# Performance work log

Hardware: AMD Instinct MI355X
Metric: run time of the kernel (lower is better)

Reference implementation:

```python
import jax, jax.numpy as jnp
import numpy as np

B, C, N, K, E = 8, 64, 4096, 16, 64
EPS = 1e-5


def _bn(h, gamma, beta, axes):
    # BatchNorm in training mode: stats over batch+spatial axes, per channel (dim 1)
    m = jnp.mean(h, axis=axes, keepdims=True)
    v = jnp.var(h, axis=axes, keepdims=True)
    shape = (1, -1) + (1,) * (h.ndim - 2)
    return gamma.reshape(shape) * (h - m) * jax.lax.rsqrt(v + EPS) + beta.reshape(shape)


def setup_inputs() -> dict:
    key = jax.random.key(0)
    ks = jax.random.split(key, 8)
    x = jax.random.normal(ks[0], (B, C, N), dtype=jnp.float32)
    idx = jax.random.randint(ks[1], (B, N, K), 0, N, dtype=jnp.int32)
    s1 = 1.0 / np.sqrt(C)
    s2 = 1.0 / np.sqrt(E)
    return {
        "x": x,
        "idx": idx,
        "W1": jax.random.normal(ks[2], (E, C), jnp.float32) * s1,
        "b1": jnp.zeros((E,), jnp.float32),
        "g1": jnp.ones((E,), jnp.float32),
        "be1": jnp.zeros((E,), jnp.float32),
        "W2": jax.random.normal(ks[3], (E, E), jnp.float32) * s2,
        "b2": jnp.zeros((E,), jnp.float32),
        "g2": jnp.ones((E,), jnp.float32),
        "be2": jnp.zeros((E,), jnp.float32),
        "W3": jax.random.normal(ks[4], (E, E), jnp.float32) * s2,
        "b3": jnp.zeros((E,), jnp.float32),
        "g3": jnp.ones((E,), jnp.float32),
        "be3": jnp.zeros((E,), jnp.float32),
    }


def reference(x, idx, W1, b1, g1, be1, W2, b2, g2, be2, W3, b3, g3, be3):
    # gather kNN neighbor features: x[b, :, idx[b]] -> (B, C, N, K)
    nn_feat = jax.vmap(lambda xb, ib: xb[:, ib])(x, idx)
    # edge features: neighbor - center
    h = nn_feat - x[..., None]                                   # (B, C, N, K)
    # Conv2DBlock: two 1x1 conv + BN + ReLU layers
    h = jnp.einsum('bcnk,oc->bonk', h, W1) + b1[:, None, None]
    h = jax.nn.relu(_bn(h, g1, be1, (0, 2, 3)))
    h = jnp.einsum('bcnk,oc->bonk', h, W2) + b2[:, None, None]
    h = jax.nn.relu(_bn(h, g2, be2, (0, 2, 3)))
    # max over neighbors
    h = jnp.max(h, axis=-1)                                      # (B, E, N)
    # Conv1DBlock: 1x1 conv + BN + ReLU
    h = jnp.einsum('bcn,oc->bon', h, W3) + b3[:, None]
    h = jax.nn.relu(_bn(h, g3, be3, (0, 2)))
    return h
```

## Files before the change

kernel.cpp:

```cpp
#include <hip/hip_runtime.h>

#define EPSBN 1e-5f
#define CNT1 524288.0f
#define CNT3 32768.0f
#define NREP 16

typedef short v8s __attribute__((ext_vector_type(8)));
typedef float v16f __attribute__((ext_vector_type(16)));

__device__ __forceinline__ unsigned short f2bf(float f) {
  union { float f; unsigned u; } v; v.f = f;
  unsigned u = v.u;
  u += 0x7fffu + ((u >> 16) & 1u);
  return (unsigned short)(u >> 16);
}
__device__ __forceinline__ unsigned pack2bf(float a, float b) {
  return (unsigned)f2bf(a) | ((unsigned)f2bf(b) << 16);
}
__device__ __forceinline__ float bflo(unsigned u) {
  union { unsigned u; float f; } v; v.u = u << 16; return v.f;
}
__device__ __forceinline__ float bfhi(unsigned u) {
  union { unsigned u; float f; } v; v.u = u & 0xffff0000u; return v.f;
}

__global__ __launch_bounds__(256) void prep(
    const float* __restrict__ x, const float* __restrict__ W1,
    unsigned short* __restrict__ y) {
  __shared__ unsigned short ldsX[64 * 72];
  int blk = blockIdx.x, t = threadIdx.x;
  int b = blk >> 6, n0 = (blk & 63) << 6;
  int tn = t & 63, cg = t >> 6;
#pragma unroll
  for (int i = 0; i < 16; ++i) {
    int c = cg * 16 + i;
    ldsX[tn * 72 + c] = f2bf(x[(((size_t)(b * 64 + c)) << 12) + n0 + tn]);
  }
  __syncthreads();
  int lane = t & 63, w = t >> 6;
  int l31 = lane & 31, lh = lane >> 5;
  int ot = w & 1, ph = w >> 1;
  int o = ot * 32 + l31;
  v16f acc;
#pragma unroll
  for (int i = 0; i < 16; ++i) acc[i] = 0.f;
#pragma unroll
  for (int ks = 0; ks < 4; ++ks) {
    const float* wrow = W1 + o * 64 + ks * 16 + lh * 8;
    float4 wa = *((const float4*)wrow);
    float4 wb = *((const float4*)(wrow + 4));
    v8s wf; unsigned* wu = (unsigned*)&wf;
    wu[0] = pack2bf(wa.x, wa.y); wu[1] = pack2bf(wa.z, wa.w);
    wu[2] = pack2bf(wb.x, wb.y); wu[3] = pack2bf(wb.z, wb.w);
    v8s af = *((const v8s*)&ldsX[(ph * 32 + l31) * 72 + ks * 16 + lh * 8]);
    acc = __builtin_amdgcn_mfma_f32_32x32x16_bf16(af, wf, acc, 0, 0, 0);
  }
#pragma unroll
  for (int i = 0; i < 16; ++i) {
    int row = (i & 3) + ((i >> 2) << 3) + (lh << 2);
    int pt = (b << 12) + n0 + ph * 32 + row;
    y[pt * 64 + o] = f2bf(acc[i]);
  }
}

__global__ __launch_bounds__(256) void p1_stats(
    const unsigned short* __restrict__ y, const int* __restrict__ idx,
    float* __restrict__ S1) {
  __shared__ float bs[64], bq[64];
  int t = threadIdx.x;
  if (t < 64) { bs[t] = 0.f; bq[t] = 0.f; }
  __syncthreads();
  int blk = blockIdx.x;
  int batch = blk & 7, bi = blk >> 3;
  int w = t >> 6, lane = t & 63;
  int ch = (lane & 7) << 3, eg = lane >> 3;
  int ebase = (batch << 16) + bi * 512 + w * 128;
  float ss[8], sq[8];
#pragma unroll
  for (int k = 0; k < 8; ++k) { ss[k] = 0.f; sq[k] = 0.f; }
  for (int it = 0; it < 16; ++it) {
    int p = ebase + it * 8 + eg;
    int j = idx[p];
    int site = p >> 4;
    uint4 uj = *((const uint4*)(y + (((size_t)((batch << 12) + j)) << 6) + ch));
    uint4 ui = *((const uint4*)(y + (((size_t)site) << 6) + ch));
    const unsigned* aj = (const unsigned*)&uj;
    const unsigned* ai = (const unsigned*)&ui;
#pragma unroll
    for (int d = 0; d < 4; ++d) {
      float d0 = bflo(aj[d]) - bflo(ai[d]);
      float d1 = bfhi(aj[d]) - bfhi(ai[d]);
      ss[2 * d] += d0; sq[2 * d] += d0 * d0;
      ss[2 * d + 1] += d1; sq[2 * d + 1] += d1 * d1;
    }
  }
#pragma unroll
  for (int k = 0; k < 8; ++k) {
    ss[k] += __shfl_xor(ss[k], 8);  sq[k] += __shfl_xor(sq[k], 8);
    ss[k] += __shfl_xor(ss[k], 16); sq[k] += __shfl_xor(sq[k], 16);
    ss[k] += __shfl_xor(ss[k], 32); sq[k] += __shfl_xor(sq[k], 32);
  }
  if (lane < 8) {
#pragma unroll
    for (int k = 0; k < 8; ++k) {
      atomicAdd(&bs[ch + k], ss[k]);
      atomicAdd(&bq[ch + k], sq[k]);
    }
  }
  __syncthreads();
  int rep = (blk >> 3) & (NREP - 1);
  if (t < 64) atomicAdd(&S1[rep * 128 + t], bs[t]);
  else if (t < 128) atomicAdd(&S1[rep * 128 + t], bq[t - 64]);
}

__global__ __launch_bounds__(256) void p2_main(
    const unsigned short* __restrict__ y, const int* __restrict__ idx,
    const float* __restrict__ W2f,
    const float* __restrict__ g1, const float* __restrict__ be1,
    const float* __restrict__ S1,
    unsigned short* __restrict__ mnb, unsigned short* __restrict__ mxb,
    float* __restrict__ S2) {
  __shared__ float bs[64], bq[64];
  __shared__ __align__(16) float lA[64];
  __shared__ __align__(16) float lC[64];
  int t = threadIdx.x;
  if (t < 64) {
    bs[t] = 0.f; bq[t] = 0.f;
    float s = 0.f, q = 0.f;
#pragma unroll
    for (int r = 0; r < NREP; ++r) { s += S1[r * 128 + t]; q += S1[r * 128 + 64 + t]; }
    float mean = s / CNT1;
    float var = q / CNT1 - mean * mean;
    float a = g1[t] * rsqrtf(var + EPSBN);
    lA[t] = a; lC[t] = be1[t] - mean * a;
  }
  __syncthreads();
  int blk = blockIdx.x;
  int batch = blk & 7, bi = blk >> 3;
  int w = t >> 6, lane = t & 63;
  int l31 = lane & 31, lh = lane >> 5;
  v8s w2[2][4];
#pragma unroll
  for (int s = 0; s < 2; ++s)
#pragma unroll
    for (int ks = 0; ks < 4; ++ks) {
      const float* wr = W2f + (s * 32 + l31) * 64 + ks * 16 + lh * 8;
      float4 wa = *((const float4*)wr);
      float4 wb = *((const float4*)(wr + 4));
      unsigned* wu = (unsigned*)&w2[s][ks];
      wu[0] = pack2bf(wa.x, wa.y); wu[1] = pack2bf(wa.z, wa.w);
      wu[2] = pack2bf(wb.x, wb.y); wu[3] = pack2bf(wb.z, wb.w);
    }
  float ss0 = 0.f, sq0 = 0.f, ss1 = 0.f, sq1 = 0.f;
  for (int it = 0; it < 8; ++it) {
    int tile = bi * 32 + w * 8 + it;
    int p = (batch << 16) + (tile << 5) + l31;
    int j = idx[p];
    int site = p >> 4;
    const unsigned short* yj = y + (((size_t)((batch << 12) + j)) << 6) + lh * 8;
    const unsigned short* yi = y + (((size_t)site) << 6) + lh * 8;
    v16f b0, b1;
#pragma unroll
    for (int i = 0; i < 16; ++i) { b0[i] = 0.f; b1[i] = 0.f; }
#pragma unroll
    for (int ks = 0; ks < 4; ++ks) {
      uint4 uj = *((const uint4*)(yj + ks * 16));
      uint4 ui = *((const uint4*)(yi + ks * 16));
      float4 a0 = *((const float4*)&lA[ks * 16 + lh * 8]);
      float4 a1 = *((const float4*)&lA[ks * 16 + lh * 8 + 4]);
      float4 c0 = *((const float4*)&lC[ks * 16 + lh * 8]);
      float4 c1 = *((const float4*)&lC[ks * 16 + lh * 8 + 4]);
      float av[8] = {a0.x, a0.y, a0.z, a0.w, a1.x, a1.y, a1.z, a1.w};
      float cv[8] = {c0.x, c0.y, c0.z, c0.w, c1.x, c1.y, c1.z, c1.w};
      const unsigned* jw = (const unsigned*)&uj;
      const unsigned* iw = (const unsigned*)&ui;
      v8s af; unsigned* au = (unsigned*)&af;
#pragma unroll
      for (int d = 0; d < 4; ++d) {
        float e0 = fmaxf((bflo(jw[d]) - bflo(iw[d])) * av[2 * d] + cv[2 * d], 0.f);
        float e1 = fmaxf((bfhi(jw[d]) - bfhi(iw[d])) * av[2 * d + 1] + cv[2 * d + 1], 0.f);
        au[d] = pack2bf(e0, e1);
      }
      b0 = __builtin_amdgcn_mfma_f32_32x32x16_bf16(af, w2[0][ks], b0, 0, 0, 0);
      b1 = __builtin_amdgcn_mfma_f32_32x32x16_bf16(af, w2[1][ks], b1, 0, 0, 0);
    }
    float mx00 = b0[0], mn00 = b0[0], mx01 = b0[8], mn01 = b0[8];
    float mx10 = b1[0], mn10 = b1[0], mx11 = b1[8], mn11 = b1[8];
#pragma unroll
    for (int i = 0; i < 16; ++i) {
      ss0 += b0[i]; sq0 += b0[i] * b0[i];
      ss1 += b1[i]; sq1 += b1[i] * b1[i];
    }
#pragma unroll
    for (int i = 1; i < 8; ++i) {
      mx00 = fmaxf(mx00, b0[i]);     mn00 = fminf(mn00, b0[i]);
      mx01 = fmaxf(mx01, b0[8 + i]); mn01 = fminf(mn01, b0[8 + i]);
      mx10 = fmaxf(mx10, b1[i]);     mn10 = fminf(mn10, b1[i]);
      mx11 = fmaxf(mx11, b1[8 + i]); mn11 = fminf(mn11, b1[8 + i]);
    }
    mx00 = fmaxf(mx00, __shfl_xor(mx00, 32)); mn00 = fminf(mn00, __shfl_xor(mn00, 32));
    mx01 = fmaxf(mx01, __shfl_xor(mx01, 32)); mn01 = fminf(mn01, __shfl_xor(mn01, 32));
    mx10 = fmaxf(mx10, __shfl_xor(mx10, 32)); mn10 = fminf(mn10, __shfl_xor(mn10, 32));
    mx11 = fmaxf(mx11, __shfl_xor(mx11, 32)); mn11 = fminf(mn11, __shfl_xor(mn11, 32));
    int s2 = (batch << 12) + (tile << 1);
    if (lh == 0) {
      mnb[(size_t)(s2 + 0) * 64 + l31] = f2bf(mn00);
      mnb[(size_t)(s2 + 1) * 64 + l31] = f2bf(mn01);
      mnb[(size_t)(s2 + 0) * 64 + 32 + l31] = f2bf(mn10);
      mnb[(size_t)(s2 + 1) * 64 + 32 + l31] = f2bf(mn11);
    } else {
      mxb[(size_t)(s2 + 0) * 64 + l31] = f2bf(mx00);
      mxb[(size_t)(s2 + 1) * 64 + l31] = f2bf(mx01);
      mxb[(size_t)(s2 + 0) * 64 + 32 + l31] = f2bf(mx10);
      mxb[(size_t)(s2 + 1) * 64 + 32 + l31] = f2bf(mx11);
    }
  }
  ss0 += __shfl_xor(ss0, 32); sq0 += __shfl_xor(sq0, 32);
  ss1 += __shfl_xor(ss1, 32); sq1 += __shfl_xor(sq1, 32);
  if (lh == 0) {
    atomicAdd(&bs[l31], ss0); atomicAdd(&bq[l31], sq0);
    atomicAdd(&bs[32 + l31], ss1); atomicAdd(&bq[32 + l31], sq1);
  }
  __syncthreads();
  int rep = blk & (NREP - 1);
  if (t < 64) atomicAdd(&S2[rep * 128 + t], bs[t]);
  else if (t < 128) atomicAdd(&S2[rep * 128 + t], bq[t - 64]);
}

__global__ __launch_bounds__(256, 2) void p3_gemm3(
    const float* __restrict__ W3f,
    const unsigned short* __restrict__ mnb, const unsigned short* __restrict__ mxb,
    const float* __restrict__ g2, const float* __restrict__ be2,
    const float* __restrict__ S2, float* __restrict__ h3, float* __restrict__ S3) {
  __shared__ uint4 ldsA[64 * 9];
  __shared__ float bs[64], bq[64], lA[64], lC[64];
  int t = threadIdx.x;
  if (t < 64) {
    bs[t] = 0.f; bq[t] = 0.f;
    float s = 0.f, q = 0.f;
#pragma unroll
    for (int r = 0; r < NREP; ++r) { s += S2[r * 128 + t]; q += S2[r * 128 + 64 + t]; }
    float mean = s / CNT1;
    float var = q / CNT1 - mean * mean;
    float a = g2[t] * rsqrtf(var + EPSBN);
    lA[t] = a; lC[t] = be2[t] - mean * a;
  }
  __syncthreads();
  int lane = t & 63, wid = t >> 6;
  int rb = wid & 1, ctile = wid >> 1;
  int l31 = lane & 31, lh = lane >> 5;
  int o = ctile * 32 + l31;
  v8s wf[4];
#pragma unroll
  for (int ks = 0; ks < 4; ++ks) {
    const float* wr = W3f + o * 64 + ks * 16 + lh * 8;
    float4 wa = *((const float4*)wr);
    float4 wb = *((const float4*)(wr + 4));
    unsigned* wu = (unsigned*)&wf[ks];
    wu[0] = pack2bf(wa.x, wa.y); wu[1] = pack2bf(wa.z, wa.w);
    wu[2] = pack2bf(wb.x, wb.y); wu[3] = pack2bf(wb.z, wb.w);
  }
  int r = t >> 2, q = t & 3;
  int arow = rb * 32 + l31;
  int s0 = blockIdx.x << 6;
  {
    int site = s0 + r;
    const uint4* mnp = (const uint4*)(mnb + (size_t)site * 64 + q * 16);
    const uint4* mxp = (const uint4*)(mxb + (size_t)site * 64 + q * 16);
    uint4 m0 = mnp[0], m1 = mnp[1], x0 = mxp[0], x1 = mxp[1];
    uint4 ch2[2];
    unsigned* cu = (unsigned*)ch2;
#pragma unroll
    for (int d = 0; d < 8; ++d) {
      unsigned md = (d < 4) ? ((const unsigned*)&m0)[d] : ((const unsigned*)&m1)[d - 4];
      unsigned xd = (d < 4) ? ((const unsigned*)&x0)[d] : ((const unsigned*)&x1)[d - 4];
      int c = q * 16 + 2 * d;
      float a0 = lA[c], a1 = lA[c + 1];
      float s0v = (a0 > 0.f) ? bflo(xd) : bflo(md);
      float s1v = (a1 > 0.f) ? bfhi(xd) : bfhi(md);
      float v0 = fmaxf(a0 * s0v + lC[c], 0.f);
      float v1 = fmaxf(a1 * s1v + lC[c + 1], 0.f);
      cu[d] = pack2bf(v0, v1);
    }
    ldsA[r * 9 + q * 2 + 0] = ch2[0];
    ldsA[r * 9 + q * 2 + 1] = ch2[1];
  }
  __syncthreads();
  v16f acc;
#pragma unroll
  for (int i = 0; i < 16; ++i) acc[i] = 0.f;
#pragma unroll
  for (int ks = 0; ks < 4; ++ks) {
    v8s a = *((const v8s*)&ldsA[arow * 9 + ks * 2 + lh]);
    acc = __builtin_amdgcn_mfma_f32_32x32x16_bf16(a, wf[ks], acc, 0, 0, 0);
  }
  float ssum = 0.f, ssq = 0.f;
#pragma unroll
  for (int i = 0; i < 16; ++i) {
    float vv = acc[i];
    ssum += vv; ssq += vv * vv;
    int row = (i & 3) + ((i >> 2) << 3) + (lh << 2);
    h3[(((size_t)(s0 + rb * 32 + row)) << 6) + o] = vv;
  }
  ssum += __shfl_xor(ssum, 32);
  ssq += __shfl_xor(ssq, 32);
  if (lh == 0) { atomicAdd(&bs[o], ssum); atomicAdd(&bq[o], ssq); }
  __syncthreads();
  int rep = blockIdx.x & (NREP - 1);
  if (t < 64) atomicAdd(&S3[rep * 128 + t], bs[t]);
  else if (t < 128) atomicAdd(&S3[rep * 128 + t], bq[t - 64]);
}

__global__ void k4_out(const float* __restrict__ h3,
                       const float* __restrict__ g3, const float* __restrict__ be3,
                       float* __restrict__ out, const float* __restrict__ S3) {
  __shared__ float lA[64], lC[64];
  __shared__ float tile[64][65];
  int t = threadIdx.x;
  if (t < 64) {
    float s = 0.f, q = 0.f;
#pragma unroll
    for (int r = 0; r < NREP; ++r) { s += S3[r * 128 + t]; q += S3[r * 128 + 64 + t]; }
    float mean = s / CNT3;
    float var = q / CNT3 - mean * mean;
    float a = g3[t] * rsqrtf(var + EPSBN);
    lA[t] = a; lC[t] = be3[t] - mean * a;
  }
  __syncthreads();
  int blk = blockIdx.x;
  int b = blk >> 6, n0 = (blk & 63) << 6;
  int r = t >> 2, q = t & 3;
  const float4* hp = (const float4*)(h3 + (((size_t)((b << 12) + n0 + r)) << 6)) + q * 4;
#pragma unroll
  for (int ii = 0; ii < 4; ++ii) {
    float4 v = hp[ii];
    int c = q * 16 + ii * 4;
    tile[c + 0][r] = fmaxf(v.x * lA[c + 0] + lC[c + 0], 0.f);
    tile[c + 1][r] = fmaxf(v.y * lA[c + 1] + lC[c + 1], 0.f);
    tile[c + 2][r] = fmaxf(v.z * lA[c + 2] + lC[c + 2], 0.f);
    tile[c + 3][r] = fmaxf(v.w * lA[c + 3] + lC[c + 3], 0.f);
  }
  __syncthreads();
  int oo = t >> 2, seg = t & 3;
  float4* dst = (float4*)(out + (((size_t)(b * 64 + oo)) << 12) + n0 + seg * 16);
#pragma unroll
  for (int ii = 0; ii < 4; ++ii) {
    float4 v;
    v.x = tile[oo][seg * 16 + ii * 4 + 0];
    v.y = tile[oo][seg * 16 + ii * 4 + 1];
    v.z = tile[oo][seg * 16 + ii * 4 + 2];
    v.w = tile[oo][seg * 16 + ii * 4 + 3];
    dst[ii] = v;
  }
}

extern "C" void kernel_launch(void* const* d_in, const int* in_sizes, int n_in,
                              void* d_out, int out_size, void* d_ws, size_t ws_size,
                              hipStream_t stream) {
  const float* x = (const float*)d_in[0];
  const int* idx = (const int*)d_in[1];
  const float* W1 = (const float*)d_in[2];
  const float* g1 = (const float*)d_in[4];
  const float* be1 = (const float*)d_in[5];
  const float* W2 = (const float*)d_in[6];
  const float* g2 = (const float*)d_in[8];
  const float* be2 = (const float*)d_in[9];
  const float* W3 = (const float*)d_in[10];
  const float* g3 = (const float*)d_in[12];
  const float* be3 = (const float*)d_in[13];
  float* out = (float*)d_out;

  char* ws = (char*)d_ws;
  unsigned short* y   = (unsigned short*)ws;
  unsigned short* mnb = (unsigned short*)(ws + (4u << 20));
  unsigned short* mxb = (unsigned short*)(ws + (8u << 20));
  float* h3           = (float*)(ws + (12u << 20));
  float* stats        = (float*)(ws + (20u << 20));
  float* S1 = stats;
  float* S2 = stats + NREP * 128;
  float* S3 = stats + 2 * NREP * 128;

  hipMemsetAsync(stats, 0, 3 * NREP * 128 * sizeof(float), stream);
  prep<<<512, 256, 0, stream>>>(x, W1, y);
  p1_stats<<<1024, 256, 0, stream>>>(y, idx, S1);
  p2_main<<<512, 256, 0, stream>>>(y, idx, W2, g1, be1, S1, mnb, mxb, S2);
  p3_gemm3<<<512, 256, 0, stream>>>(W3, mnb, mxb, g2, be2, S2, h3, S3);
  k4_out<<<512, 256, 0, stream>>>(h3, g3, be3, out, S3);
}
```

Before: 140.9 us.

## Fuse five kernels into one persistent cooperative kernel with grid syncs

```diff
diff --git a/kernel.cpp b/kernel.cpp
--- a/kernel.cpp
+++ b/kernel.cpp
@@ -1,4 +1,7 @@
 #include <hip/hip_runtime.h>
+#include <hip/hip_cooperative_groups.h>
+
+namespace cg = cooperative_groups;
 
 #define EPSBN 1e-5f
 #define CNT1 524288.0f
@@ -24,74 +27,83 @@
   union { unsigned u; float f; } v; v.u = u & 0xffff0000u; return v.f;
 }
 
-__global__ __launch_bounds__(256) void prep(
-    const float* __restrict__ x, const float* __restrict__ W1,
-    unsigned short* __restrict__ y) {
-  __shared__ unsigned short ldsX[64 * 72];
-  int blk = blockIdx.x, t = threadIdx.x;
-  int b = blk >> 6, n0 = (blk & 63) << 6;
-  int tn = t & 63, cg = t >> 6;
-#pragma unroll
-  for (int i = 0; i < 16; ++i) {
-    int c = cg * 16 + i;
-    ldsX[tn * 72 + c] = f2bf(x[(((size_t)(b * 64 + c)) << 12) + n0 + tn]);
-  }
-  __syncthreads();
+
+__device__ __forceinline__ void phase0(
+    int nb, const float* __restrict__ x, const float* __restrict__ W1f,
+    unsigned short* __restrict__ y, float* __restrict__ stats, char* lds) {
+  int t = threadIdx.x;
+  for (int i = blockIdx.x * 256 + t; i < 3 * NREP * 128; i += nb * 256)
+    stats[i] = 0.f;
+  unsigned short* ldsX = (unsigned short*)lds;
   int lane = t & 63, w = t >> 6;
   int l31 = lane & 31, lh = lane >> 5;
   int ot = w & 1, ph = w >> 1;
   int o = ot * 32 + l31;
-  v16f acc;
-#pragma unroll
-  for (int i = 0; i < 16; ++i) acc[i] = 0.f;
+  v8s wfr[4];
 #pragma unroll
   for (int ks = 0; ks < 4; ++ks) {
-    const float* wrow = W1 + o * 64 + ks * 16 + lh * 8;
+    const float* wrow = W1f + o * 64 + ks * 16 + lh * 8;
     float4 wa = *((const float4*)wrow);
     float4 wb = *((const float4*)(wrow + 4));
-    v8s wf; unsigned* wu = (unsigned*)&wf;
+    unsigned* wu = (unsigned*)&wfr[ks];
     wu[0] = pack2bf(wa.x, wa.y); wu[1] = pack2bf(wa.z, wa.w);
     wu[2] = pack2bf(wb.x, wb.y); wu[3] = pack2bf(wb.z, wb.w);
-    v8s af = *((const v8s*)&ldsX[(ph * 32 + l31) * 72 + ks * 16 + lh * 8]);
-    acc = __builtin_amdgcn_mfma_f32_32x32x16_bf16(af, wf, acc, 0, 0, 0);
-  }
-#pragma unroll
-  for (int i = 0; i < 16; ++i) {
-    int row = (i & 3) + ((i >> 2) << 3) + (lh << 2);
-    int pt = (b << 12) + n0 + ph * 32 + row;
-    y[pt * 64 + o] = f2bf(acc[i]);
-  }
-}
-
-__global__ __launch_bounds__(256) void p1_stats(
-    const unsigned short* __restrict__ y, const int* __restrict__ idx,
-    float* __restrict__ S1) {
-  __shared__ float bs[64], bq[64];
+  }
+  for (int u = blockIdx.x; u < 512; u += nb) {
+    int b = u >> 6, n0 = (u & 63) << 6;
+#pragma unroll
+    for (int i = 0; i < 16; ++i) {
+      int c = w * 16 + i;
+      ldsX[lane * 72 + c] = f2bf(x[(((size_t)(b * 64 + c)) << 12) + n0 + lane]);
+    }
+    __syncthreads();
+    v16f acc;
+#pragma unroll
+    for (int i = 0; i < 16; ++i) acc[i] = 0.f;
+#pragma unroll
+    for (int ks = 0; ks < 4; ++ks) {
+      v8s af = *((const v8s*)&ldsX[(ph * 32 + l31) * 72 + ks * 16 + lh * 8]);
+      acc = __builtin_amdgcn_mfma_f32_32x32x16_bf16(af, wfr[ks], acc, 0, 0, 0);
+    }
+#pragma unroll
+    for (int i = 0; i < 16; ++i) {
+      int row = (i & 3) + ((i >> 2) << 3) + (lh << 2);
+      int pt = (b << 12) + n0 + ph * 32 + row;
+      y[pt * 64 + o] = f2bf(acc[i]);
+    }
+    __syncthreads();
+  }
+}
+
+__device__ __forceinline__ void phase1(
+    int nb, const unsigned short* __restrict__ y, const int* __restrict__ idx,
+    float* __restrict__ S1, float* bs, float* bq) {
   int t = threadIdx.x;
   if (t < 64) { bs[t] = 0.f; bq[t] = 0.f; }
   __syncthreads();
-  int blk = blockIdx.x;
-  int batch = blk & 7, bi = blk >> 3;
-  int w = t >> 6, lane = t & 63;
+  int lane = t & 63, w = t >> 6;
   int ch = (lane & 7) << 3, eg = lane >> 3;
-  int ebase = (batch << 16) + bi * 512 + w * 128;
   float ss[8], sq[8];
 #pragma unroll
   for (int k = 0; k < 8; ++k) { ss[k] = 0.f; sq[k] = 0.f; }
-  for (int it = 0; it < 16; ++it) {
-    int p = ebase + it * 8 + eg;
-    int j = idx[p];
-    int site = p >> 4;
-    uint4 uj = *((const uint4*)(y + (((size_t)((batch << 12) + j)) << 6) + ch));
-    uint4 ui = *((const uint4*)(y + (((size_t)site) << 6) + ch));
-    const unsigned* aj = (const unsigned*)&uj;
-    const unsigned* ai = (const unsigned*)&ui;
-#pragma unroll
-    for (int d = 0; d < 4; ++d) {
-      float d0 = bflo(aj[d]) - bflo(ai[d]);
-      float d1 = bfhi(aj[d]) - bfhi(ai[d]);
-      ss[2 * d] += d0; sq[2 * d] += d0 * d0;
-      ss[2 * d + 1] += d1; sq[2 * d + 1] += d1 * d1;
+  for (int u = blockIdx.x; u < 512; u += nb) {
+    int batch = u & 7, bi = u >> 3;
+    int ebase = (batch << 16) + bi * 1024 + w * 256;
+    for (int it = 0; it < 32; ++it) {
+      int p = ebase + it * 8 + eg;
+      int j = idx[p];
+      int site = p >> 4;
+      uint4 uj = *((const uint4*)(y + (((size_t)((batch << 12) + j)) << 6) + ch));
+      uint4 ui = *((const uint4*)(y + (((size_t)site) << 6) + ch));
+      const unsigned* aj = (const unsigned*)&uj;
+      const unsigned* ai = (const unsigned*)&ui;
+#pragma unroll
+      for (int d = 0; d < 4; ++d) {
+        float d0 = bflo(aj[d]) - bflo(ai[d]);
+        float d1 = bfhi(aj[d]) - bfhi(ai[d]);
+        ss[2 * d] += d0; sq[2 * d] += d0 * d0;
+        ss[2 * d + 1] += d1; sq[2 * d + 1] += d1 * d1;
+      }
     }
   }
 #pragma unroll
@@ -108,24 +120,19 @@
     }
   }
   __syncthreads();
-  int rep = (blk >> 3) & (NREP - 1);
+  int rep = blockIdx.x & (NREP - 1);
   if (t < 64) atomicAdd(&S1[rep * 128 + t], bs[t]);
   else if (t < 128) atomicAdd(&S1[rep * 128 + t], bq[t - 64]);
 }
 
-__global__ __launch_bounds__(256) void p2_main(
-    const unsigned short* __restrict__ y, const int* __restrict__ idx,
-    const float* __restrict__ W2f,
-    const float* __restrict__ g1, const float* __restrict__ be1,
-    const float* __restrict__ S1,
+__device__ __forceinline__ void phase2(
+    int nb, const unsigned short* __restrict__ y, const int* __restrict__ idx,
+    const float* __restrict__ W2f, const float* __restrict__ g1,
+    const float* __restrict__ be1, const float* __restrict__ S1,
     unsigned short* __restrict__ mnb, unsigned short* __restrict__ mxb,
-    float* __restrict__ S2) {
-  __shared__ float bs[64], bq[64];
-  __shared__ __align__(16) float lA[64];
-  __shared__ __align__(16) float lC[64];
+    float* __restrict__ S2, float* bs, float* bq, float* lA, float* lC) {
   int t = threadIdx.x;
   if (t < 64) {
-    bs[t] = 0.f; bq[t] = 0.f;
     float s = 0.f, q = 0.f;
 #pragma unroll
     for (int r = 0; r < NREP; ++r) { s += S1[r * 128 + t]; q += S1[r * 128 + 64 + t]; }
@@ -133,11 +140,10 @@
     float var = q / CNT1 - mean * mean;
     float a = g1[t] * rsqrtf(var + EPSBN);
     lA[t] = a; lC[t] = be1[t] - mean * a;
-  }
-  __syncthreads();
-  int blk = blockIdx.x;
-  int batch = blk & 7, bi = blk >> 3;
-  int w = t >> 6, lane = t & 63;
+    bs[t] = 0.f; bq[t] = 0.f;
+  }
+  __syncthreads();
+  int lane = t & 63, w = t >> 6;
   int l31 = lane & 31, lh = lane >> 5;
   v8s w2[2][4];
 #pragma unroll
@@ -152,67 +158,70 @@
       wu[2] = pack2bf(wb.x, wb.y); wu[3] = pack2bf(wb.z, wb.w);
     }
   float ss0 = 0.f, sq0 = 0.f, ss1 = 0.f, sq1 = 0.f;
-  for (int it = 0; it < 8; ++it) {
-    int tile = bi * 32 + w * 8 + it;
-    int p = (batch << 16) + (tile << 5) + l31;
-    int j = idx[p];
-    int site = p >> 4;
-    const unsigned short* yj = y + (((size_t)((batch << 12) + j)) << 6) + lh * 8;
-    const unsigned short* yi = y + (((size_t)site) << 6) + lh * 8;
-    v16f b0, b1;
-#pragma unroll
-    for (int i = 0; i < 16; ++i) { b0[i] = 0.f; b1[i] = 0.f; }
-#pragma unroll
-    for (int ks = 0; ks < 4; ++ks) {
-      uint4 uj = *((const uint4*)(yj + ks * 16));
-      uint4 ui = *((const uint4*)(yi + ks * 16));
-      float4 a0 = *((const float4*)&lA[ks * 16 + lh * 8]);
-      float4 a1 = *((const float4*)&lA[ks * 16 + lh * 8 + 4]);
-      float4 c0 = *((const float4*)&lC[ks * 16 + lh * 8]);
-      float4 c1 = *((const float4*)&lC[ks * 16 + lh * 8 + 4]);
-      float av[8] = {a0.x, a0.y, a0.z, a0.w, a1.x, a1.y, a1.z, a1.w};
-      float cv[8] = {c0.x, c0.y, c0.z, c0.w, c1.x, c1.y, c1.z, c1.w};
-      const unsigned* jw = (const unsigned*)&uj;
-      const unsigned* iw = (const unsigned*)&ui;
-      v8s af; unsigned* au = (unsigned*)&af;
-#pragma unroll
-      for (int d = 0; d < 4; ++d) {
-        float e0 = fmaxf((bflo(jw[d]) - bflo(iw[d])) * av[2 * d] + cv[2 * d], 0.f);
-        float e1 = fmaxf((bfhi(jw[d]) - bfhi(iw[d])) * av[2 * d + 1] + cv[2 * d + 1], 0.f);
-        au[d] = pack2bf(e0, e1);
-      }
-      b0 = __builtin_amdgcn_mfma_f32_32x32x16_bf16(af, w2[0][ks], b0, 0, 0, 0);
-      b1 = __builtin_amdgcn_mfma_f32_32x32x16_bf16(af, w2[1][ks], b1, 0, 0, 0);
-    }
-    float mx00 = b0[0], mn00 = b0[0], mx01 = b0[8], mn01 = b0[8];
-    float mx10 = b1[0], mn10 = b1[0], mx11 = b1[8], mn11 = b1[8];
-#pragma unroll
-    for (int i = 0; i < 16; ++i) {
-      ss0 += b0[i]; sq0 += b0[i] * b0[i];
-      ss1 += b1[i]; sq1 += b1[i] * b1[i];
-    }
-#pragma unroll
-    for (int i = 1; i < 8; ++i) {
-      mx00 = fmaxf(mx00, b0[i]);     mn00 = fminf(mn00, b0[i]);
-      mx01 = fmaxf(mx01, b0[8 + i]); mn01 = fminf(mn01, b0[8 + i]);
-      mx10 = fmaxf(mx10, b1[i]);     mn10 = fminf(mn10, b1[i]);
-      mx11 = fmaxf(mx11, b1[8 + i]); mn11 = fminf(mn11, b1[8 + i]);
-    }
-    mx00 = fmaxf(mx00, __shfl_xor(mx00, 32)); mn00 = fminf(mn00, __shfl_xor(mn00, 32));
-    mx01 = fmaxf(mx01, __shfl_xor(mx01, 32)); mn01 = fminf(mn01, __shfl_xor(mn01, 32));
-    mx10 = fmaxf(mx10, __shfl_xor(mx10, 32)); mn10 = fminf(mn10, __shfl_xor(mn10, 32));
-    mx11 = fmaxf(mx11, __shfl_xor(mx11, 32)); mn11 = fminf(mn11, __shfl_xor(mn11, 32));
-    int s2 = (batch << 12) + (tile << 1);
-    if (lh == 0) {
-      mnb[(size_t)(s2 + 0) * 64 + l31] = f2bf(mn00);
-      mnb[(size_t)(s2 + 1) * 64 + l31] = f2bf(mn01);
-      mnb[(size_t)(s2 + 0) * 64 + 32 + l31] = f2bf(mn10);
-      mnb[(size_t)(s2 + 1) * 64 + 32 + l31] = f2bf(mn11);
-    } else {
-      mxb[(size_t)(s2 + 0) * 64 + l31] = f2bf(mx00);
-      mxb[(size_t)(s2 + 1) * 64 + l31] = f2bf(mx01);
-      mxb[(size_t)(s2 + 0) * 64 + 32 + l31] = f2bf(mx10);
-      mxb[(size_t)(s2 + 1) * 64 + 32 + l31] = f2bf(mx11);
+  for (int u = blockIdx.x; u < 512; u += nb) {
+    int batch = u & 7, bi = u >> 3;
+    for (int it = 0; it < 8; ++it) {
+      int tile = bi * 32 + w * 8 + it;
+      int p = (batch << 16) + (tile << 5) + l31;
+      int j = idx[p];
+      int site = p >> 4;
+      const unsigned short* yj = y + (((size_t)((batch << 12) + j)) << 6) + lh * 8;
+      const unsigned short* yi = y + (((size_t)site) << 6) + lh * 8;
+      v16f b0, b1;
+#pragma unroll
+      for (int i = 0; i < 16; ++i) { b0[i] = 0.f; b1[i] = 0.f; }
+#pragma unroll
+      for (int ks = 0; ks < 4; ++ks) {
+        uint4 uj = *((const uint4*)(yj + ks * 16));
+        uint4 ui = *((const uint4*)(yi + ks * 16));
+        float4 a0 = *((const float4*)&lA[ks * 16 + lh * 8]);
+        float4 a1 = *((const float4*)&lA[ks * 16 + lh * 8 + 4]);
+        float4 c0 = *((const float4*)&lC[ks * 16 + lh * 8]);
+        float4 c1 = *((const float4*)&lC[ks * 16 + lh * 8 + 4]);
+        float av[8] = {a0.x, a0.y, a0.z, a0.w, a1.x, a1.y, a1.z, a1.w};
+        float cv[8] = {c0.x, c0.y, c0.z, c0.w, c1.x, c1.y, c1.z, c1.w};
+        const unsigned* jw = (const unsigned*)&uj;
+        const unsigned* iw = (const unsigned*)&ui;
+        v8s af; unsigned* au = (unsigned*)&af;
+#pragma unroll
+        for (int d = 0; d < 4; ++d) {
+          float e0 = fmaxf((bflo(jw[d]) - bflo(iw[d])) * av[2 * d] + cv[2 * d], 0.f);
+          float e1 = fmaxf((bfhi(jw[d]) - bfhi(iw[d])) * av[2 * d + 1] + cv[2 * d + 1], 0.f);
+          au[d] = pack2bf(e0, e1);
+        }
+        b0 = __builtin_amdgcn_mfma_f32_32x32x16_bf16(af, w2[0][ks], b0, 0, 0, 0);
+        b1 = __builtin_amdgcn_mfma_f32_32x32x16_bf16(af, w2[1][ks], b1, 0, 0, 0);
+      }
+      float mx00 = b0[0], mn00 = b0[0], mx01 = b0[8], mn01 = b0[8];
+      float mx10 = b1[0], mn10 = b1[0], mx11 = b1[8], mn11 = b1[8];
+#pragma unroll
+      for (int i = 0; i < 16; ++i) {
+        ss0 += b0[i]; sq0 += b0[i] * b0[i];
+        ss1 += b1[i]; sq1 += b1[i] * b1[i];
+      }
+#pragma unroll
+      for (int i = 1; i < 8; ++i) {
+        mx00 = fmaxf(mx00, b0[i]);     mn00 = fminf(mn00, b0[i]);
+        mx01 = fmaxf(mx01, b0[8 + i]); mn01 = fminf(mn01, b0[8 + i]);
+        mx10 = fmaxf(mx10, b1[i]);     mn10 = fminf(mn10, b1[i]);
+        mx11 = fmaxf(mx11, b1[8 + i]); mn11 = fminf(mn11, b1[8 + i]);
+      }
+      mx00 = fmaxf(mx00, __shfl_xor(mx00, 32)); mn00 = fminf(mn00, __shfl_xor(mn00, 32));
+      mx01 = fmaxf(mx01, __shfl_xor(mx01, 32)); mn01 = fminf(mn01, __shfl_xor(mn01, 32));
+      mx10 = fmaxf(mx10, __shfl_xor(mx10, 32)); mn10 = fminf(mn10, __shfl_xor(mn10, 32));
+      mx11 = fmaxf(mx11, __shfl_xor(mx11, 32)); mn11 = fminf(mn11, __shfl_xor(mn11, 32));
+      int s2 = (batch << 12) + (tile << 1);
+      if (lh == 0) {
+        mnb[(size_t)(s2 + 0) * 64 + l31] = f2bf(mn00);
+        mnb[(size_t)(s2 + 1) * 64 + l31] = f2bf(mn01);
+        mnb[(size_t)(s2 + 0) * 64 + 32 + l31] = f2bf(mn10);
+        mnb[(size_t)(s2 + 1) * 64 + 32 + l31] = f2bf(mn11);
+      } else {
+        mxb[(size_t)(s2 + 0) * 64 + l31] = f2bf(mx00);
+        mxb[(size_t)(s2 + 1) * 64 + l31] = f2bf(mx01);
+        mxb[(size_t)(s2 + 0) * 64 + 32 + l31] = f2bf(mx10);
+        mxb[(size_t)(s2 + 1) * 64 + 32 + l31] = f2bf(mx11);
+      }
     }
   }
   ss0 += __shfl_xor(ss0, 32); sq0 += __shfl_xor(sq0, 32);
@@ -222,21 +231,20 @@
     atomicAdd(&bs[32 + l31], ss1); atomicAdd(&bq[32 + l31], sq1);
   }
   __syncthreads();
-  int rep = blk & (NREP - 1);
+  int rep = blockIdx.x & (NREP - 1);
   if (t < 64) atomicAdd(&S2[rep * 128 + t], bs[t]);
   else if (t < 128) atomicAdd(&S2[rep * 128 + t], bq[t - 64]);
 }
 
-__global__ __launch_bounds__(256, 2) void p3_gemm3(
-    const float* __restrict__ W3f,
-    const unsigned short* __restrict__ mnb, const unsigned short* __restrict__ mxb,
-    const float* __restrict__ g2, const float* __restrict__ be2,
-    const float* __restrict__ S2, float* __restrict__ h3, float* __restrict__ S3) {
-  __shared__ uint4 ldsA[64 * 9];
-  __shared__ float bs[64], bq[64], lA[64], lC[64];
+__device__ __forceinline__ void phase3(
+    int nb, const float* __restrict__ W3f, const unsigned short* __restrict__ mnb,
+    const unsigned short* __restrict__ mxb, const float* __restrict__ g2,
+    const float* __restrict__ be2, const float* __restrict__ S2,
+    float* __restrict__ h3, float* __restrict__ S3,
+    float* bs, float* bq, float* lA, float* lC, char* lds) {
+  uint4* ldsA = (uint4*)lds;
   int t = threadIdx.x;
   if (t < 64) {
-    bs[t] = 0.f; bq[t] = 0.f;
     float s = 0.f, q = 0.f;
 #pragma unroll
     for (int r = 0; r < NREP; ++r) { s += S2[r * 128 + t]; q += S2[r * 128 + 64 + t]; }
@@ -244,11 +252,12 @@
     float var = q / CNT1 - mean * mean;
     float a = g2[t] * rsqrtf(var + EPSBN);
     lA[t] = a; lC[t] = be2[t] - mean * a;
-  }
-  __syncthreads();
-  int lane = t & 63, wid = t >> 6;
-  int rb = wid & 1, ctile = wid >> 1;
+    bs[t] = 0.f; bq[t] = 0.f;
+  }
+  __syncthreads();
+  int lane = t & 63, w = t >> 6;
   int l31 = lane & 31, lh = lane >> 5;
+  int rb = w & 1, ctile = w >> 1;
   int o = ctile * 32 + l31;
   v8s wf[4];
 #pragma unroll
@@ -262,45 +271,48 @@
   }
   int r = t >> 2, q = t & 3;
   int arow = rb * 32 + l31;
-  int s0 = blockIdx.x << 6;
-  {
-    int site = s0 + r;
-    const uint4* mnp = (const uint4*)(mnb + (size_t)site * 64 + q * 16);
-    const uint4* mxp = (const uint4*)(mxb + (size_t)site * 64 + q * 16);
-    uint4 m0 = mnp[0], m1 = mnp[1], x0 = mxp[0], x1 = mxp[1];
-    uint4 ch2[2];
-    unsigned* cu = (unsigned*)ch2;
-#pragma unroll
-    for (int d = 0; d < 8; ++d) {
-      unsigned md = (d < 4) ? ((const unsigned*)&m0)[d] : ((const unsigned*)&m1)[d - 4];
-      unsigned xd = (d < 4) ? ((const unsigned*)&x0)[d] : ((const unsigned*)&x1)[d - 4];
-      int c = q * 16 + 2 * d;
-      float a0 = lA[c], a1 = lA[c + 1];
-      float s0v = (a0 > 0.f) ? bflo(xd) : bflo(md);
-      float s1v = (a1 > 0.f) ? bfhi(xd) : bfhi(md);
-      float v0 = fmaxf(a0 * s0v + lC[c], 0.f);
-      float v1 = fmaxf(a1 * s1v + lC[c + 1], 0.f);
-      cu[d] = pack2bf(v0, v1);
-    }
-    ldsA[r * 9 + q * 2 + 0] = ch2[0];
-    ldsA[r * 9 + q * 2 + 1] = ch2[1];
-  }
-  __syncthreads();
-  v16f acc;
-#pragma unroll
-  for (int i = 0; i < 16; ++i) acc[i] = 0.f;
-#pragma unroll
-  for (int ks = 0; ks < 4; ++ks) {
-    v8s a = *((const v8s*)&ldsA[arow * 9 + ks * 2 + lh]);
-    acc = __builtin_amdgcn_mfma_f32_32x32x16_bf16(a, wf[ks], acc, 0, 0, 0);
-  }
   float ssum = 0.f, ssq = 0.f;
-#pragma unroll
-  for (int i = 0; i < 16; ++i) {
-    float vv = acc[i];
-    ssum += vv; ssq += vv * vv;
-    int row = (i & 3) + ((i >> 2) << 3) + (lh << 2);
-    h3[(((size_t)(s0 + rb * 32 + row)) << 6) + o] = vv;
+  for (int u = blockIdx.x; u < 512; u += nb) {
+    int s0 = u << 6;
+    {
+      int site = s0 + r;
+      const uint4* mnp = (const uint4*)(mnb + (size_t)site * 64 + q * 16);
+      const uint4* mxp = (const uint4*)(mxb + (size_t)site * 64 + q * 16);
+      uint4 m0 = mnp[0], m1 = mnp[1], x0 = mxp[0], x1 = mxp[1];
+      uint4 ch2[2];
+      unsigned* cu = (unsigned*)ch2;
+#pragma unroll
+      for (int d = 0; d < 8; ++d) {
+        unsigned md = (d < 4) ? ((const unsigned*)&m0)[d] : ((const unsigned*)&m1)[d - 4];
+        unsigned xd = (d < 4) ? ((const unsigned*)&x0)[d] : ((const unsigned*)&x1)[d - 4];
+        int c = q * 16 + 2 * d;
+        float a0 = lA[c], a1 = lA[c + 1];
+        float s0v = (a0 > 0.f) ? bflo(xd) : bflo(md);
+        float s1v = (a1 > 0.f) ? bfhi(xd) : bfhi(md);
+        float v0 = fmaxf(a0 * s0v + lC[c], 0.f);
+        float v1 = fmaxf(a1 * s1v + lC[c + 1], 0.f);
+        cu[d] = pack2bf(v0, v1);
+      }
+      ldsA[r * 9 + q * 2 + 0] = ch2[0];
+      ldsA[r * 9 + q * 2 + 1] = ch2[1];
+    }
+    __syncthreads();
+    v16f acc;
+#pragma unroll
+    for (int i = 0; i < 16; ++i) acc[i] = 0.f;
+#pragma unroll
+    for (int ks = 0; ks < 4; ++ks) {
+      v8s a = *((const v8s*)&ldsA[arow * 9 + ks * 2 + lh]);
+      acc = __builtin_amdgcn_mfma_f32_32x32x16_bf16(a, wf[ks], acc, 0, 0, 0);
+    }
+#pragma unroll
+    for (int i = 0; i < 16; ++i) {
+      float vv = acc[i];
+      ssum += vv; ssq += vv * vv;
+      int row = (i & 3) + ((i >> 2) << 3) + (lh << 2);
+      h3[(((size_t)(s0 + rb * 32 + row)) << 6) + o] = vv;
+    }
+    __syncthreads();
   }
   ssum += __shfl_xor(ssum, 32);
   ssq += __shfl_xor(ssq, 32);
@@ -311,11 +323,11 @@
   else if (t < 128) atomicAdd(&S3[rep * 128 + t], bq[t - 64]);
 }
 
-__global__ void k4_out(const float* __restrict__ h3,
-                       const float* __restrict__ g3, const float* __restrict__ be3,
-                       float* __restrict__ out, const float* __restrict__ S3) {
-  __shared__ float lA[64], lC[64];
-  __shared__ float tile[64][65];
+__device__ __forceinline__ void phase4(
+    int nb, const float* __restrict__ h3, const float* __restrict__ g3,
+    const float* __restrict__ be3, const float* __restrict__ S3,
+    float* __restrict__ out, float* lA, float* lC, char* lds) {
+  float* tile = (float*)lds;
   int t = threadIdx.x;
   if (t < 64) {
     float s = 0.f, q = 0.f;
@@ -327,31 +339,98 @@
     lA[t] = a; lC[t] = be3[t] - mean * a;
   }
   __syncthreads();
-  int blk = blockIdx.x;
-  int b = blk >> 6, n0 = (blk & 63) << 6;
   int r = t >> 2, q = t & 3;
-  const float4* hp = (const float4*)(h3 + (((size_t)((b << 12) + n0 + r)) << 6)) + q * 4;
-#pragma unroll
-  for (int ii = 0; ii < 4; ++ii) {
-    float4 v = hp[ii];
-    int c = q * 16 + ii * 4;
-    tile[c + 0][r] = fmaxf(v.x * lA[c + 0] + lC[c + 0], 0.f);
-    tile[c + 1][r] = fmaxf(v.y * lA[c + 1] + lC[c + 1], 0.f);
-    tile[c + 2][r] = fmaxf(v.z * lA[c + 2] + lC[c + 2], 0.f);
-    tile[c + 3][r] = fmaxf(v.w * lA[c + 3] + lC[c + 3], 0.f);
-  }
-  __syncthreads();
-  int oo = t >> 2, seg = t & 3;
-  float4* dst = (float4*)(out + (((size_t)(b * 64 + oo)) << 12) + n0 + seg * 16);
-#pragma unroll
-  for (int ii = 0; ii < 4; ++ii) {
-    float4 v;
-    v.x = tile[oo][seg * 16 + ii * 4 + 0];
-    v.y = tile[oo][seg * 16 + ii * 4 + 1];
-    v.z = tile[oo][seg * 16 + ii * 4 + 2];
-    v.w = tile[oo][seg * 16 + ii * 4 + 3];
-    dst[ii] = v;
-  }
+  for (int u = blockIdx.x; u < 512; u += nb) {
+    int b = u >> 6, n0 = (u & 63) << 6;
+    const float4* hp = (const float4*)(h3 + (((size_t)((b << 12) + n0 + r)) << 6)) + q * 4;
+#pragma unroll
+    for (int ii = 0; ii < 4; ++ii) {
+      float4 v = hp[ii];
+      int c = q * 16 + ii * 4;
+      tile[(c + 0) * 65 + r] = fmaxf(v.x * lA[c + 0] + lC[c + 0], 0.f);
+      tile[(c + 1) * 65 + r] = fmaxf(v.y * lA[c + 1] + lC[c + 1], 0.f);
+      tile[(c + 2) * 65 + r] = fmaxf(v.z * lA[c + 2] + lC[c + 2], 0.f);
+      tile[(c + 3) * 65 + r] = fmaxf(v.w * lA[c + 3] + lC[c + 3], 0.f);
+    }
+    __syncthreads();
+    int oo = t >> 2, seg = t & 3;
+    float4* dst = (float4*)(out + (((size_t)(b * 64 + oo)) << 12) + n0 + seg * 16);
+#pragma unroll
+    for (int ii = 0; ii < 4; ++ii) {
+      float4 v;
+      v.x = tile[oo * 65 + seg * 16 + ii * 4 + 0];
+      v.y = tile[oo * 65 + seg * 16 + ii * 4 + 1];
+      v.z = tile[oo * 65 + seg * 16 + ii * 4 + 2];
+      v.w = tile[oo * 65 + seg * 16 + ii * 4 + 3];
+      dst[ii] = v;
+    }
+    __syncthreads();
+  }
+}
+
+__global__ __launch_bounds__(256, 2) void fused_all(
+    const float* x, const int* idx, const float* W1f, const float* W2f,
+    const float* W3f, const float* g1, const float* be1, const float* g2,
+    const float* be2, const float* g3, const float* be3,
+    unsigned short* y, unsigned short* mnb, unsigned short* mxb,
+    float* h3, float* stats, float* out) {
+  cg::grid_group grid = cg::this_grid();
+  __shared__ __align__(16) char lds[16640];
+  __shared__ float bs[64], bq[64];
+  __shared__ __align__(16) float lA[64];
+  __shared__ __align__(16) float lC[64];
+  int nb = gridDim.x;
+  float* S1 = stats;
+  float* S2 = stats + NREP * 128;
+  float* S3 = stats + 2 * NREP * 128;
+  phase0(nb, x, W1f, y, stats, lds);
+  grid.sync();
+  phase1(nb, y, idx, S1, bs, bq);
+  grid.sync();
+  phase2(nb, y, idx, W2f, g1, be1, S1, mnb, mxb, S2, bs, bq, lA, lC);
+  grid.sync();
+  phase3(nb, W3f, mnb, mxb, g2, be2, S2, h3, S3, bs, bq, lA, lC, lds);
+  grid.sync();
+  phase4(nb, h3, g3, be3, S3, out, lA, lC, lds);
+}
+
+__global__ __launch_bounds__(256) void k0(const float* x, const float* W1f,
+                                          unsigned short* y, float* stats) {
+  __shared__ __align__(16) char lds[9216];
+  phase0(gridDim.x, x, W1f, y, stats, lds);
+}
+__global__ __launch_bounds__(256) void k1(const unsigned short* y, const int* idx,
+                                          float* S1) {
+  __shared__ float bs[64], bq[64];
+  phase1(gridDim.x, y, idx, S1, bs, bq);
+}
+__global__ __launch_bounds__(256) void k2(const unsigned short* y, const int* idx,
+                                          const float* W2f, const float* g1,
+                                          const float* be1, const float* S1,
+                                          unsigned short* mnb, unsigned short* mxb,
+                                          float* S2) {
+  __shared__ float bs[64], bq[64];
+  __shared__ __align__(16) float lA[64];
+  __shared__ __align__(16) float lC[64];
+  phase2(gridDim.x, y, idx, W2f, g1, be1, S1, mnb, mxb, S2, bs, bq, lA, lC);
+}
+__global__ __launch_bounds__(256) void k3(const float* W3f, const unsigned short* mnb,
+                                          const unsigned short* mxb, const float* g2,
+                                          const float* be2, const float* S2,
+                                          float* h3, float* S3) {
+  __shared__ __align__(16) char lds[9216];
+  __shared__ float bs[64], bq[64];
+  __shared__ __align__(16) float lA[64];
+  __shared__ __align__(16) float lC[64];
+  phase3(gridDim.x, W3f, mnb, mxb, g2, be2, S2, h3, S3, bs, bq, lA, lC, lds);
+}
+__global__ __launch_bounds__(256) void k4(const float* h3, const float* g3,
+                                          const float* be3, const float* S3,
+                                          float* out) {
+  __shared__ __align__(16) char lds[16640];
+  __shared__ __align__(16) float lA[64];
+  __shared__ __align__(16) float lC[64];
+  phase4(gridDim.x, h3, g3, be3, S3, out, lA, lC, lds);
 }
 
 extern "C" void kernel_launch(void* const* d_in, const int* in_sizes, int n_in,
@@ -376,14 +455,42 @@
   unsigned short* mxb = (unsigned short*)(ws + (8u << 20));
   float* h3           = (float*)(ws + (12u << 20));
   float* stats        = (float*)(ws + (20u << 20));
-  float* S1 = stats;
-  float* S2 = stats + NREP * 128;
-  float* S3 = stats + 2 * NREP * 128;
-
-  hipMemsetAsync(stats, 0, 3 * NREP * 128 * sizeof(float), stream);
-  prep<<<512, 256, 0, stream>>>(x, W1, y);
-  p1_stats<<<1024, 256, 0, stream>>>(y, idx, S1);
-  p2_main<<<512, 256, 0, stream>>>(y, idx, W2, g1, be1, S1, mnb, mxb, S2);
-  p3_gemm3<<<512, 256, 0, stream>>>(W3, mnb, mxb, g2, be2, S2, h3, S3);
-  k4_out<<<512, 256, 0, stream>>>(h3, g3, be3, out, S3);
-}
+
+  bool coop_ok = false;
+  int perCU = 0;
+  hipError_t oe = hipOccupancyMaxActiveBlocksPerMultiprocessor(
+      &perCU, (const void*)fused_all, 256, 0);
+  if (oe == hipSuccess && perCU >= 1) {
+    int dev = 0;
+    (void)hipGetDevice(&dev);
+    hipDeviceProp_t prop;
+    hipError_t pe = hipGetDeviceProperties(&prop, dev);
+    int cus = (pe == hipSuccess) ? prop.multiProcessorCount : 256;
+    long grid = (long)perCU * (long)cus;
+    if (grid > 512) grid = 512;
+    if (grid >= 64) {
+      void* args[] = {(void*)&x, (void*)&idx, (void*)&W1, (void*)&W2, (void*)&W3,
+                      (void*)&g1, (void*)&be1, (void*)&g2, (void*)&be2,
+                      (void*)&g3, (void*)&be3,
+                      (void*)&y, (void*)&mnb, (void*)&mxb, (void*)&h3,
+                      (void*)&stats, (void*)&out};
+      hipError_t le = hipLaunchCooperativeKernel((const void*)fused_all,
+                                                 dim3((unsigned)grid), dim3(256),
+                                                 args, 0, stream);
+      coop_ok = (le == hipSuccess);
+      if (!coop_ok) (void)hipGetLastError();
+    }
+  } else {
+    (void)hipGetLastError();
+  }
+
+  if (!coop_ok) {
+    k0<<<512, 256, 0, stream>>>(x, W1, y, stats);
+    k1<<<512, 256, 0, stream>>>(y, idx, stats);
+    k2<<<512, 256, 0, stream>>>(y, idx, W2, g1, be1, stats, mnb, mxb,
+                                stats + NREP * 128);
+    k3<<<512, 256, 0, stream>>>(W3, mnb, mxb, g2, be2, stats + NREP * 128,
+                                h3, stats + 2 * NREP * 128);
+    k4<<<512, 256, 0, stream>>>(h3, g3, be3, stats + 2 * NREP * 128, out);
+  }
+}
```

Measured after the change: 283.4 us. 101% more time.
